# Kernel tuning notes

Measured on AMD Instinct MI355X. Metric: run time of the kernel, lower is better.

The kernel has to match this reference:

```python
import jax, jax.numpy as jnp
import numpy as np

N_E = 4096
E_DIM = 256
DECAY = 0.99
EPS = 1e-5


def setup_inputs() -> dict:
    key = jax.random.key(0)
    k1, k2 = jax.random.split(key)
    z = jax.random.normal(k1, (8, 256, 16, 16, 16), dtype=jnp.float32)
    embedding = jax.random.normal(k2, (N_E, E_DIM), dtype=jnp.float32)
    return {
        "z": z,
        "embedding": embedding,
        "cluster_size": jnp.zeros((N_E,), dtype=jnp.float32),
        "embedding_avg": embedding,  # buffer initialized as embedding.clone()
    }


def reference(z, embedding, cluster_size, embedding_avg):
    n_e, e_dim = embedding.shape
    # b c h w d -> b h w d c, then flatten tokens
    zt = jnp.einsum('bchwd->bhwdc', z)
    zf = zt.reshape(-1, e_dim)                      # [N, e_dim]
    # squared euclidean distances: ||z||^2 + ||e||^2 - 2 z.e
    d = (jnp.sum(zf * zf, axis=1, keepdims=True)
         + jnp.sum(embedding * embedding, axis=1)
         - 2.0 * jnp.einsum('bd,nd->bn', zf, embedding))  # [N, n_e]
    idx = jnp.argmin(d, axis=1)                     # [N]
    # EMA statistics (equivalent to one-hot.T reductions, done via scatter)
    n_total = jnp.zeros((n_e,), zf.dtype).at[idx].add(1.0)          # encodings.sum(0)
    dw = jax.ops.segment_sum(zf, idx, num_segments=n_e)             # encodings.T @ zf
    new_cluster = cluster_size * DECAY + (1.0 - DECAY) * n_total
    new_avg = embedding_avg * DECAY + (1.0 - DECAY) * dw
    n = new_cluster.sum()
    cs = (new_cluster + EPS) / (n + n_e * EPS) * n
    new_embed = new_avg / cs[:, None]
    # quantize (gather == one-hot @ embedding) with straight-through estimator
    zq = jnp.take(embedding, idx, axis=0).reshape(zt.shape)
    zq = zt + jax.lax.stop_gradient(zq - zt)
    zq = jnp.einsum('bhwdc->bchwd', zq)
    usage = (n_total > 0).sum().astype(jnp.float32) / n_e
    return zq, idx, new_cluster, new_avg, new_embed, usage
```

## Files before the change

### kernel.cpp

```cpp
#include <hip/hip_runtime.h>

#define N_E   4096
#define E_DIM 256
#define NTOK  32768
#define ZX    4096
#define DECAY 0.99f
#define EPSV  1e-5f
#define TAU   0.3f
#define NJB   32
#define NSPL  4
#define IBIG  0x7fffffff

typedef _Float16 half8 __attribute__((ext_vector_type(8)));
typedef __attribute__((ext_vector_type(4))) float f32x4;

__device__ __forceinline__ unsigned short f2h(float x) {
    _Float16 h = (_Float16)x;
    unsigned short u;
    __builtin_memcpy(&u, &h, 2);
    return u;
}
__device__ __forceinline__ float h2f(unsigned short u) {
    _Float16 h;
    __builtin_memcpy(&h, &u, 2);
    return (float)h;
}
__device__ __forceinline__ unsigned umin2(unsigned a, unsigned b) { return a < b ? a : b; }
__device__ __forceinline__ unsigned umax2(unsigned a, unsigned b) { return a > b ? a : b; }
__device__ __forceinline__ void gload16(const void* g, void* l) {
    __builtin_amdgcn_global_load_lds(
        (const __attribute__((address_space(1))) char*)g,
        (__attribute__((address_space(3))) char*)l, 16, 0, 0);
}

__global__ void k_prep(const float* __restrict__ z, unsigned short* __restrict__ zh,
                       const float* __restrict__ emb, unsigned short* __restrict__ Bp,
                       float* __restrict__ enorm32, double* __restrict__ enorm64,
                       int* __restrict__ cnt, int* __restrict__ flagCnt,
                       int* __restrict__ flagCnt2) {
    __shared__ float lt[64][65];
    const int tid = threadIdx.x;
    if (blockIdx.x < 2048) {
        const int bid = blockIdx.x;
        const int xt = bid & 63, ct = (bid >> 6) & 3, b = bid >> 8;
        #pragma unroll
        for (int r = 0; r < 4; ++r) {
            int cy = r * 16 + (tid >> 4);
            int xx4 = tid & 15;
            float4 v = ((const float4*)z)[(size_t)(b * 256 + ct * 64 + cy) * 1024 + xt * 16 + xx4];
            lt[cy][xx4 * 4 + 0] = v.x; lt[cy][xx4 * 4 + 1] = v.y;
            lt[cy][xx4 * 4 + 2] = v.z; lt[cy][xx4 * 4 + 3] = v.w;
        }
        __syncthreads();
        #pragma unroll
        for (int it = 0; it < 2; ++it) {
            int tl = it * 32 + (tid >> 3);
            int c8 = tid & 7;
            unsigned short h[8];
            #pragma unroll
            for (int u = 0; u < 8; ++u) h[u] = f2h(lt[c8 * 8 + u][tl]);
            size_t t = (size_t)(b * 4096 + xt * 64 + tl);
            size_t o = t * 256 + ct * 64 + c8 * 8;
            *(ushort4*)&zh[o]     = make_ushort4(h[0], h[1], h[2], h[3]);
            *(ushort4*)&zh[o + 4] = make_ushort4(h[4], h[5], h[6], h[7]);
        }
    } else {
        const int eb = blockIdx.x - 2048;
        if (tid < 4) cnt[eb * 4 + tid] = 0;
        if (eb == 0 && tid == 0) { *flagCnt = 0; *flagCnt2 = 0; }
        int j = eb * 4 + (tid >> 6);
        int lane = tid & 63;
        float4 v = ((const float4*)emb)[(size_t)j * 64 + lane];
        float f[4] = {v.x, v.y, v.z, v.w};
        unsigned short h[4];
        #pragma unroll
        for (int u = 0; u < 4; ++u) h[u] = f2h(f[u]);
        *(ushort4*)&Bp[(size_t)j * E_DIM + lane * 4] = make_ushort4(h[0], h[1], h[2], h[3]);
        double s = 0.0;
        #pragma unroll
        for (int u = 0; u < 4; ++u) s += (double)f[u] * (double)f[u];
        #pragma unroll
        for (int off = 32; off; off >>= 1) s += __shfl_down(s, off, 64);
        if (lane == 0) { enorm32[j] = (float)s; enorm64[j] = s; }
    }
}

__global__ __launch_bounds__(256) void k_dist(
        const unsigned short* __restrict__ zh,
        const unsigned short* __restrict__ Bp, const float* __restrict__ enorm32,
        unsigned* __restrict__ pk1, unsigned* __restrict__ pk2, unsigned* __restrict__ pk3) {
    __shared__ __align__(16) char smem[32768];
    const int tid = threadIdx.x;
    const int lane = tid & 63;
    const int w = tid >> 6;
    const int wr = w >> 1, wc = w & 1;
    const int t0 = blockIdx.x * 128;
    const int jb = blockIdx.y;
    const int j0 = jb * 128;
    const int sw16 = (((lane & 7) ^ (lane >> 3)) << 4);
    const int rowsub = lane >> 3;

    f32x4 acc[4][4];
    #pragma unroll
    for (int m = 0; m < 4; ++m)
        #pragma unroll
        for (int nn = 0; nn < 4; ++nn)
            acc[m][nn] = (f32x4){0.f, 0.f, 0.f, 0.f};

    auto stage = [&](int s) {
        const int kb = s * 128 + sw16;
        #pragma unroll
        for (int c = 0; c < 4; ++c) {
            int seg = w * 4 + c;
            int arow = t0 + seg * 8 + rowsub;
            int brow = j0 + seg * 8 + rowsub;
            gload16((const char*)zh + (size_t)arow * 512 + kb, &smem[seg * 1024]);
            gload16((const char*)Bp + (size_t)brow * 512 + kb, &smem[16384 + seg * 1024]);
        }
    };

    stage(0);
    for (int s = 0; s < 4; ++s) {
        __syncthreads();
        const int xr = ((lane & 7) << 4);
        #pragma unroll
        for (int kk = 0; kk < 2; ++kk) {
            const int colb = (kk * 64 + ((lane >> 4) << 4)) ^ xr;
            half8 a[4], b[4];
            #pragma unroll
            for (int m = 0; m < 4; ++m)
                a[m] = *(const half8*)&smem[((wr * 64 + m * 16 + (lane & 15)) << 7) + colb];
            #pragma unroll
            for (int nn = 0; nn < 4; ++nn)
                b[nn] = *(const half8*)&smem[16384 + ((wc * 64 + nn * 16 + (lane & 15)) << 7) + colb];
            #pragma unroll
            for (int m = 0; m < 4; ++m)
                #pragma unroll
                for (int nn = 0; nn < 4; ++nn)
                    acc[m][nn] = __builtin_amdgcn_mfma_f32_16x16x32_f16(b[nn], a[m], acc[m][nn], 0, 0, 0);
        }
        if (s < 3) {
            __syncthreads();
            stage(s + 1);
        }
    }

    const int g   = lane >> 4;
    const int gg4 = g * 4;
    const int cbase = (wc << 6);
    float enb[4][4];
    #pragma unroll
    for (int nn = 0; nn < 4; ++nn) {
        float4 e4 = *(const float4*)&enorm32[j0 + wc * 64 + nn * 16 + gg4];
        enb[nn][0] = e4.x + 4096.f; enb[nn][1] = e4.y + 4096.f;
        enb[nn][2] = e4.z + 4096.f; enb[nn][3] = e4.w + 4096.f;
    }
    unsigned s1 = 0, s2 = 0, s3 = 0;
    #pragma unroll
    for (int m = 0; m < 4; ++m) {
        unsigned k1 = 0xFFFFFFFFu, k2 = 0xFFFFFFFFu, k3 = 0xFFFFFFFFu;
        #pragma unroll
        for (int nn = 0; nn < 4; ++nn)
            #pragma unroll
            for (int r = 0; r < 4; ++r) {
                float sc = fmaf(-2.f, acc[m][nn][r], enb[nn][r]);
                unsigned key = (__float_as_uint(sc) & 0xFFFFFF80u)
                             | (unsigned)(cbase | (gg4 + nn * 16 + r));
                k3 = umin2(k3, umax2(k2, key));
                k2 = umin2(k2, umax2(k1, key));
                k1 = umin2(k1, key);
            }
        #pragma unroll
        for (int off = 16; off <= 32; off <<= 1) {
            unsigned b1 = (unsigned)__shfl_xor((int)k1, off, 64);
            unsigned b2 = (unsigned)__shfl_xor((int)k2, off, 64);
            unsigned b3 = (unsigned)__shfl_xor((int)k3, off, 64);
            unsigned p  = umax2(k1, b1);
            unsigned q  = umin2(k2, b2);
            unsigned r2 = umax2(k2, b2);
            unsigned ss = umin2(k3, b3);
            k1 = umin2(k1, b1);
            k2 = umin2(p, q);
            k3 = umin2(umax2(p, q), umin2(r2, ss));
        }
        s1 = (g == m) ? k1 : s1;
        s2 = (g == m) ? k2 : s2;
        s3 = (g == m) ? k3 : s3;
    }
    unsigned* mb = (unsigned*)smem;
    __syncthreads();
    if (wc == 1) {
        mb[wr * 64 + lane]       = s1;
        mb[128 + wr * 64 + lane] = s2;
        mb[256 + wr * 64 + lane] = s3;
    }
    __syncthreads();
    if (wc == 0) {
        unsigned o1 = mb[wr * 64 + lane];
        unsigned o2 = mb[128 + wr * 64 + lane];
        unsigned o3 = mb[256 + wr * 64 + lane];
        unsigned r1 = umin2(s1, o1);
        unsigned A  = umax2(s1, o1);
        unsigned B  = umin2(s2, o2);
        unsigned C  = umax2(s2, o2);
        unsigned D  = umin2(s3, o3);
        unsigned r2 = umin2(A, B);
        unsigned r3 = umin2(umax2(A, B), umin2(C, D));
        size_t o = (size_t)jb * NTOK + t0 + wr * 64 + lane;
        pk1[o] = r1; pk2[o] = r2; pk3[o] = r3;
    }
}

__global__ void k_merge(const unsigned* __restrict__ pk1, const unsigned* __restrict__ pk2,
                        const unsigned* __restrict__ pk3,
                        int* __restrict__ idx32, int* __restrict__ cnt,
                        float* __restrict__ out_idx,
                        int* __restrict__ xlist, int* __restrict__ xn,
                        int* __restrict__ flagList, int* __restrict__ flagCount,
                        int* __restrict__ flagList2, int* __restrict__ flagCount2) {
    int t = blockIdx.x * blockDim.x + threadIdx.x;
    if (t >= NTOK) return;
    unsigned g1 = 0xFFFFFFFFu, g2 = 0xFFFFFFFFu;
    int h1 = 0;
    #pragma unroll 4
    for (int s = 0; s < NJB; s++) {
        unsigned a = pk1[(size_t)s * NTOK + t];
        unsigned b = pk2[(size_t)s * NTOK + t];
        bool c = a < g1;
        g2 = c ? g1 : umin2(g2, a);
        h1 = c ? s : h1;
        g1 = c ? a : g1;
        g2 = umin2(g2, b);
    }
    int x1 = h1 * 128 + (int)(g1 & 127u);
    idx32[t] = x1;
    atomicAdd(&cnt[x1], 1);
    out_idx[t] = (float)x1;
    float v1 = __uint_as_float(g1 & 0xFFFFFF80u);
    float v2 = __uint_as_float(g2 & 0xFFFFFF80u);
    if (v2 - v1 >= TAU) return;
    unsigned thrk = __float_as_uint(v1 + TAU) | 127u;
    int nc = 0; bool full = false;
    for (int s = 0; s < NJB; s++) {
        unsigned a = pk1[(size_t)s * NTOK + t];
        if (a > thrk) continue;
        if (pk3[(size_t)s * NTOK + t] <= thrk) { full = true; break; }
        if (nc == 8) { full = true; break; }
        xlist[t * 8 + nc++] = s * 128 + (int)(a & 127u);
        unsigned b = pk2[(size_t)s * NTOK + t];
        if (b <= thrk) {
            if (nc == 8) { full = true; break; }
            xlist[t * 8 + nc++] = s * 128 + (int)(b & 127u);
        }
    }
    if (full) {
        int q = atomicAdd(flagCount2, 1);
        flagList2[q] = t;
    } else {
        xn[t] = nc;
        int q = atomicAdd(flagCount, 1);
        flagList[q] = t;
    }
}

__global__ __launch_bounds__(512) void k_triR(
        const float* __restrict__ z, const float* __restrict__ emb,
        const double* __restrict__ enorm64,
        const int* __restrict__ flagList, const int* __restrict__ flagCount,
        const int* __restrict__ xlist, const int* __restrict__ xn,
        const int* __restrict__ flagList2, const int* __restrict__ flagCount2,
        int* __restrict__ idx32, int* __restrict__ cnt, float* __restrict__ out_idx) {
    __shared__ float zrow[E_DIM];
    __shared__ double rv[512];
    __shared__ int ri[512];
    const int tid = threadIdx.x;
    if (blockIdx.x < 384) {
        const int lane = tid & 63;
        const int wid = blockIdx.x * 8 + (tid >> 6);
        const int nw = 384 * 8;
        const int nf = *flagCount;
        for (int f = wid; f < nf; f += nw) {
            int t = flagList[f];
            int b = t >> 12, x = t & 4095;
            double zz[4];
            #pragma unroll
            for (int u = 0; u < 4; ++u)
                zz[u] = (double)z[(size_t)(b * 256 + lane * 4 + u) * 4096 + x];
            int m = xn[t];
            double best = 1e300; int bi = IBIG;
            for (int c = 0; c < m; ++c) {
                int j = xlist[t * 8 + c];
                float4 e = ((const float4*)emb)[(size_t)j * 64 + lane];
                double d = zz[0] * (double)e.x + zz[1] * (double)e.y
                         + zz[2] * (double)e.z + zz[3] * (double)e.w;
                #pragma unroll
                for (int off = 32; off; off >>= 1) d += __shfl_down(d, off, 64);
                double s = enorm64[j] - 2.0 * d;
                if (s < best || (s == best && j < bi)) { best = s; bi = j; }
            }
            if (lane == 0) {
                int old = idx32[t];
                if (bi != old) {
                    idx32[t] = bi;
                    out_idx[t] = (float)bi;
                    atomicSub(&cnt[old], 1);
                    atomicAdd(&cnt[bi], 1);
                }
            }
        }
    } else {
        const int nf = *flagCount2;
        for (int f = blockIdx.x - 384; f < nf; f += 128) {
            const int t = flagList2[f];
            const int b = t >> 12, x = t & 4095;
            __syncthreads();
            if (tid < E_DIM) zrow[tid] = z[(size_t)(b * 256 + tid) * 4096 + x];
            __syncthreads();
            double best = 1e300; int bi = IBIG;
            for (int s = 0; s < N_E / 512; s++) {
                int j = s * 512 + tid;
                const float4* er4 = (const float4*)(emb + (size_t)j * E_DIM);
                double a0 = 0.0, a1 = 0.0, a2 = 0.0, a3 = 0.0;
                for (int k4 = 0; k4 < 64; ++k4) {
                    float4 e = er4[k4];
                    a0 = fma((double)e.x, (double)zrow[k4 * 4 + 0], a0);
                    a1 = fma((double)e.y, (double)zrow[k4 * 4 + 1], a1);
                    a2 = fma((double)e.z, (double)zrow[k4 * 4 + 2], a2);
                    a3 = fma((double)e.w, (double)zrow[k4 * 4 + 3], a3);
                }
                double d = enorm64[j] - 2.0 * ((a0 + a1) + (a2 + a3));
                if (d < best || (d == best && j < bi)) { best = d; bi = j; }
            }
            rv[tid] = best; ri[tid] = bi;
            __syncthreads();
            for (int off = 256; off; off >>= 1) {
                if (tid < off) {
                    if (rv[tid + off] < rv[tid] ||
                        (rv[tid + off] == rv[tid] && ri[tid + off] < ri[tid])) {
                        rv[tid] = rv[tid + off]; ri[tid] = ri[tid + off];
                    }
                }
                __syncthreads();
            }
            if (tid == 0) {
                int old = idx32[t];
                int nw2 = ri[0];
                if (nw2 != old) {
                    idx32[t] = nw2;
                    out_idx[t] = (float)nw2;
                    atomicSub(&cnt[old], 1);
                    atomicAdd(&cnt[nw2], 1);
                }
            }
            __syncthreads();
        }
    }
}

__global__ void k_scan(const int* __restrict__ cnt, int* __restrict__ offs,
                       const float* __restrict__ cluster_size,
                       float* __restrict__ nval, float* __restrict__ out_usage) {
    __shared__ int sc[1024];
    __shared__ float sn[1024];
    __shared__ float su[1024];
    int tid = threadIdx.x;
    int c0 = cnt[tid * 4], c1 = cnt[tid * 4 + 1], c2 = cnt[tid * 4 + 2], c3 = cnt[tid * 4 + 3];
    int ls = c0 + c1 + c2 + c3;
    float ns = 0.f, us = 0.f;
    {
        int cc[4] = {c0, c1, c2, c3};
        #pragma unroll
        for (int u = 0; u < 4; ++u) {
            ns += cluster_size[tid * 4 + u] * DECAY + (1.f - DECAY) * (float)cc[u];
            us += (cc[u] > 0) ? 1.f : 0.f;
        }
    }
    sc[tid] = ls; sn[tid] = ns; su[tid] = us;
    __syncthreads();
    for (int off = 1; off < 1024; off <<= 1) {
        int v = (tid >= off) ? sc[tid - off] : 0;
        __syncthreads();
        sc[tid] += v;
        __syncthreads();
    }
    int base = sc[tid] - ls;
    offs[tid * 4] = base;
    offs[tid * 4 + 1] = base + c0;
    offs[tid * 4 + 2] = base + c0 + c1;
    offs[tid * 4 + 3] = base + c0 + c1 + c2;
    for (int off = 512; off; off >>= 1) {
        if (tid < off) { sn[tid] += sn[tid + off]; su[tid] += su[tid + off]; }
        __syncthreads();
    }
    if (tid == 0) { *nval = sn[0]; *out_usage = su[0] / (float)N_E; }
}

__global__ void k_place(const int* __restrict__ idx32, int* __restrict__ offs,
                        int* __restrict__ tokList) {
    int t = blockIdx.x * blockDim.x + threadIdx.x;
    if (t >= NTOK) return;
    int j = idx32[t];
    int p = atomicAdd(&offs[j], 1);
    tokList[p] = t;
}

__global__ __launch_bounds__(512) void k_dwzq(const unsigned short* __restrict__ zh,
                       const int* __restrict__ cnt, const int* __restrict__ offs,
                       const int* __restrict__ tokList, float* __restrict__ dwp,
                       const float* __restrict__ emb, const int* __restrict__ idx32,
                       float* __restrict__ out_zq) {
    __shared__ float red[8][256];
    if (blockIdx.x < N_E) {
        const int j = blockIdx.x;
        const int split = blockIdx.y;
        const int g = threadIdx.x >> 6;
        const int lane = threadIdx.x & 63;
        const int n = cnt[j];
        const int s0 = offs[j] - n;
        const int stride = NSPL * 8;
        float4 acc = make_float4(0.f, 0.f, 0.f, 0.f);
        int i = split * 8 + g;
        if (i < n) {
            int t_cur = tokList[s0 + i];
            i += stride;
            for (; i < n; i += stride) {
                int t_nxt = tokList[s0 + i];
                ushort4 h = *(const ushort4*)&zh[(size_t)t_cur * 256 + lane * 4];
                acc.x += h2f(h.x); acc.y += h2f(h.y);
                acc.z += h2f(h.z); acc.w += h2f(h.w);
                t_cur = t_nxt;
            }
            ushort4 h = *(const ushort4*)&zh[(size_t)t_cur * 256 + lane * 4];
            acc.x += h2f(h.x); acc.y += h2f(h.y);
            acc.z += h2f(h.z); acc.w += h2f(h.w);
        }
        red[g][lane * 4 + 0] = acc.x; red[g][lane * 4 + 1] = acc.y;
        red[g][lane * 4 + 2] = acc.z; red[g][lane * 4 + 3] = acc.w;
        __syncthreads();
        if (g == 0) {
            float4 o;
            int c = lane * 4;
            o.x = red[0][c+0] + red[1][c+0] + red[2][c+0] + red[3][c+0]
                + red[4][c+0] + red[5][c+0] + red[6][c+0] + red[7][c+0];
            o.y = red[0][c+1] + red[1][c+1] + red[2][c+1] + red[3][c+1]
                + red[4][c+1] + red[5][c+1] + red[6][c+1] + red[7][c+1];
            o.z = red[0][c+2] + red[1][c+2] + red[2][c+2] + red[3][c+2]
                + red[4][c+2] + red[5][c+2] + red[6][c+2] + red[7][c+2];
            o.w = red[0][c+3] + red[1][c+3] + red[2][c+3] + red[3][c+3]
                + red[4][c+3] + red[5][c+3] + red[6][c+3] + red[7][c+3];
            ((float4*)dwp)[((size_t)split * N_E + j) * 64 + lane] = o;
        }
    } else {
        int t = (blockIdx.x - N_E) * (NSPL * 512) + blockIdx.y * 512 + threadIdx.x;
        int j = idx32[t];
        int b = t >> 12, x = t & 4095;
        const float4* er = (const float4*)(emb + (size_t)j * E_DIM);
        float* ob = out_zq + (size_t)b * (E_DIM * ZX) + x;
        #pragma unroll 8
        for (int c4 = 0; c4 < E_DIM / 4; c4++) {
            float4 v = er[c4];
            ob[(size_t)(c4 * 4 + 0) * ZX] = v.x;
            ob[(size_t)(c4 * 4 + 1) * ZX] = v.y;
            ob[(size_t)(c4 * 4 + 2) * ZX] = v.z;
            ob[(size_t)(c4 * 4 + 3) * ZX] = v.w;
        }
    }
}

__global__ void k_final(const float* __restrict__ dwp, const int* __restrict__ cnt,
                        const float* __restrict__ cluster_size,
                        const float* __restrict__ emb_avg, const float* __restrict__ nval,
                        float* __restrict__ out_cluster, float* __restrict__ out_avg,
                        float* __restrict__ out_embed) {
    int j = blockIdx.x * 4 + (threadIdx.x >> 6);
    int lane = threadIdx.x & 63;
    float4 dw = make_float4(0.f, 0.f, 0.f, 0.f);
    #pragma unroll
    for (int s = 0; s < NSPL; ++s) {
        float4 v = ((const float4*)dwp)[((size_t)s * N_E + j) * 64 + lane];
        dw.x += v.x; dw.y += v.y; dw.z += v.z; dw.w += v.w;
    }
    float nc = cluster_size[j] * DECAY + (1.f - DECAY) * (float)cnt[j];
    float nv = *nval;
    float cs = (nc + EPSV) / (nv + (float)N_E * EPSV) * nv;
    float4 ea = ((const float4*)emb_avg)[(size_t)j * 64 + lane];
    float4 na, ne;
    na.x = ea.x * DECAY + (1.f - DECAY) * dw.x;
    na.y = ea.y * DECAY + (1.f - DECAY) * dw.y;
    na.z = ea.z * DECAY + (1.f - DECAY) * dw.z;
    na.w = ea.w * DECAY + (1.f - DECAY) * dw.w;
    ne.x = na.x / cs; ne.y = na.y / cs; ne.z = na.z / cs; ne.w = na.w / cs;
    ((float4*)out_avg)[(size_t)j * 64 + lane] = na;
    ((float4*)out_embed)[(size_t)j * 64 + lane] = ne;
    if (lane == 0) out_cluster[j] = nc;
}

extern "C" void kernel_launch(void* const* d_in, const int* in_sizes, int n_in,
                              void* d_out, int out_size, void* d_ws, size_t ws_size,
                              hipStream_t stream) {
    const float* z            = (const float*)d_in[0];
    const float* emb          = (const float*)d_in[1];
    const float* cluster_size = (const float*)d_in[2];
    const float* emb_avg      = (const float*)d_in[3];
    float* out = (float*)d_out;

    char* ws = (char*)d_ws;
    unsigned short* zh   = (unsigned short*)(ws + 0);
    float* enorm32       = (float*)(ws + 16777216);
    double* enorm64      = (double*)(ws + 16793600);
    int* idx32           = (int*)(ws + 16826368);
    int* flagList        = (int*)(ws + 16957440);
    int* flagList2       = (int*)(ws + 17088512);
    int* xlist           = (int*)(ws + 17219584);
    int* xn              = (int*)(ws + 18268160);
    int* cnt             = (int*)(ws + 18399232);
    int* offs            = (int*)(ws + 18415616);
    int* flagCnt         = (int*)(ws + 18432000);
    int* flagCnt2        = (int*)(ws + 18432064);
    float* nval          = (float*)(ws + 18432128);
    float* dwp           = (float*)(ws + 18874368);
    int*   tokList       = (int*)(ws + 35651584);

    unsigned* pk1        = (unsigned*)(out + 0);
    unsigned* pk2        = (unsigned*)(out + 1048576);
    unsigned* pk3        = (unsigned*)(out + 2097152);
    unsigned short* Bp   = (unsigned short*)(out + 3145728);

    float* out_zq      = out + 0;
    float* out_idx     = out + 8388608;
    float* out_cluster = out + 8421376;
    float* out_avg     = out + 8425472;
    float* out_embed   = out + 9474048;
    float* out_usage   = out + 10522624;

    hipLaunchKernelGGL(k_prep,   dim3(3072), dim3(256), 0, stream,
                       z, zh, emb, Bp, enorm32, enorm64, cnt, flagCnt, flagCnt2);
    hipLaunchKernelGGL(k_dist,   dim3(256, NJB), dim3(256), 0, stream,
                       zh, Bp, enorm32, pk1, pk2, pk3);
    hipLaunchKernelGGL(k_merge,  dim3(128), dim3(256), 0, stream,
                       pk1, pk2, pk3, idx32, cnt, out_idx,
                       xlist, xn, flagList, flagCnt, flagList2, flagCnt2);
    hipLaunchKernelGGL(k_triR,   dim3(512), dim3(512), 0, stream,
                       z, emb, enorm64, flagList, flagCnt, xlist, xn,
                       flagList2, flagCnt2, idx32, cnt, out_idx);
    hipLaunchKernelGGL(k_scan,   dim3(1), dim3(1024), 0, stream, cnt, offs,
                       cluster_size, nval, out_usage);
    hipLaunchKernelGGL(k_place,  dim3(128), dim3(256), 0, stream, idx32, offs, tokList);
    hipLaunchKernelGGL(k_dwzq,   dim3(N_E + 16, NSPL), dim3(512), 0, stream,
                       zh, cnt, offs, tokList, dwp, emb, idx32, out_zq);
    hipLaunchKernelGGL(k_final,  dim3(1024), dim3(256), 0, stream,
                       dwp, cnt, cluster_size, emb_avg, nval,
                       out_cluster, out_avg, out_embed);
}
```

Measured before the change: 201.8 us.

## Double-buffer distance GEMM K-loop with thinner K-steps and single barrier

Restructures the k_dist main loop from four 128-byte K-stages with two syncthreads each into eight 64-byte K-stages that ping-pong between two 16KB LDS buffers. The next stage is prefetched asynchronously while MFMAs run on the current one, and each iteration ends with one waitcnt plus barrier. The LDS layout and swizzle change so two rows share a 128-byte line. The aim is to overlap global-to-LDS loads with compute and cut barrier count, at the cost of more loop iterations with fewer MFMAs each.

```diff
diff --git a/kernel.cpp b/kernel.cpp
--- a/kernel.cpp
+++ b/kernel.cpp
@@ -97,8 +97,28 @@
     const int t0 = blockIdx.x * 128;
     const int jb = blockIdx.y;
     const int j0 = jb * 128;
-    const int sw16 = (((lane & 7) ^ (lane >> 3)) << 4);
-    const int rowsub = lane >> 3;
+
+    int rowc[2], slotc[2];
+    #pragma unroll
+    for (int c = 0; c < 2; ++c) {
+        int q = c * 256 + tid;
+        int rp = q >> 3, pos = q & 7;
+        int posx = pos ^ (rp & 7);
+        rowc[c] = rp * 2 + (posx >> 2);
+        slotc[c] = posx & 3;
+    }
+    const char* aS0 = (const char*)zh + (size_t)(t0 + rowc[0]) * 512 + slotc[0] * 16;
+    const char* aS1 = (const char*)zh + (size_t)(t0 + rowc[1]) * 512 + slotc[1] * 16;
+    const char* bS0 = (const char*)Bp + (size_t)(j0 + rowc[0]) * 512 + slotc[0] * 16;
+    const char* bS1 = (const char*)Bp + (size_t)(j0 + rowc[1]) * 512 + slotc[1] * 16;
+
+    const int g = lane >> 4;
+    const int r0a = wr * 64 + (lane & 15);
+    const int r0b = wc * 64 + (lane & 15);
+    const int posxA = (g | ((r0a & 1) << 2)) ^ ((r0a >> 1) & 7);
+    const int posxB = (g | ((r0b & 1) << 2)) ^ ((r0b >> 1) & 7);
+    const int Aoff = (r0a >> 1) * 128 + posxA * 16;
+    const int Boff = (r0b >> 1) * 128 + posxB * 16;
 
     f32x4 acc[4][4];
     #pragma unroll
@@ -107,46 +127,40 @@
         for (int nn = 0; nn < 4; ++nn)
             acc[m][nn] = (f32x4){0.f, 0.f, 0.f, 0.f};
 
-    auto stage = [&](int s) {
-        const int kb = s * 128 + sw16;
-        #pragma unroll
-        for (int c = 0; c < 4; ++c) {
-            int seg = w * 4 + c;
-            int arow = t0 + seg * 8 + rowsub;
-            int brow = j0 + seg * 8 + rowsub;
-            gload16((const char*)zh + (size_t)arow * 512 + kb, &smem[seg * 1024]);
-            gload16((const char*)Bp + (size_t)brow * 512 + kb, &smem[16384 + seg * 1024]);
-        }
+    auto stage = [&](int s, int buf) {
+        char* dst = smem + buf * 16384;
+        gload16(aS0 + s * 64, dst + w * 1024);
+        gload16(aS1 + s * 64, dst + 4096 + w * 1024);
+        gload16(bS0 + s * 64, dst + 8192 + w * 1024);
+        gload16(bS1 + s * 64, dst + 12288 + w * 1024);
     };
 
-    stage(0);
-    for (int s = 0; s < 4; ++s) {
-        __syncthreads();
-        const int xr = ((lane & 7) << 4);
-        #pragma unroll
-        for (int kk = 0; kk < 2; ++kk) {
-            const int colb = (kk * 64 + ((lane >> 4) << 4)) ^ xr;
-            half8 a[4], b[4];
-            #pragma unroll
-            for (int m = 0; m < 4; ++m)
-                a[m] = *(const half8*)&smem[((wr * 64 + m * 16 + (lane & 15)) << 7) + colb];
+    stage(0, 0);
+    asm volatile("s_waitcnt vmcnt(0)" ::: "memory");
+    __builtin_amdgcn_s_barrier();
+    #pragma unroll 1
+    for (int s = 0; s < 8; ++s) {
+        const int buf = s & 1;
+        if (s < 7) stage(s + 1, buf ^ 1);
+        const int base = buf * 16384;
+        half8 a[4], b[4];
+        #pragma unroll
+        for (int m = 0; m < 4; ++m)
+            a[m] = *(const half8*)&smem[base + Aoff + m * 1024];
+        #pragma unroll
+        for (int nn = 0; nn < 4; ++nn)
+            b[nn] = *(const half8*)&smem[base + 8192 + Boff + nn * 1024];
+        #pragma unroll
+        for (int m = 0; m < 4; ++m)
             #pragma unroll
             for (int nn = 0; nn < 4; ++nn)
-                b[nn] = *(const half8*)&smem[16384 + ((wc * 64 + nn * 16 + (lane & 15)) << 7) + colb];
-            #pragma unroll
-            for (int m = 0; m < 4; ++m)
-                #pragma unroll
-                for (int nn = 0; nn < 4; ++nn)
-                    acc[m][nn] = __builtin_amdgcn_mfma_f32_16x16x32_f16(b[nn], a[m], acc[m][nn], 0, 0, 0);
-        }
-        if (s < 3) {
-            __syncthreads();
-            stage(s + 1);
-        }
-    }
-
-    const int g   = lane >> 4;
-    const int gg4 = g * 4;
+                acc[m][nn] = __builtin_amdgcn_mfma_f32_16x16x32_f16(b[nn], a[m], acc[m][nn], 0, 0, 0);
+        asm volatile("s_waitcnt vmcnt(0)" ::: "memory");
+        __builtin_amdgcn_s_barrier();
+    }
+
+    const int gq  = lane >> 4;
+    const int gg4 = gq * 4;
     const int cbase = (wc << 6);
     float enb[4][4];
     #pragma unroll
@@ -183,12 +197,11 @@
             k2 = umin2(p, q);
             k3 = umin2(umax2(p, q), umin2(r2, ss));
         }
-        s1 = (g == m) ? k1 : s1;
-        s2 = (g == m) ? k2 : s2;
-        s3 = (g == m) ? k3 : s3;
+        s1 = (gq == m) ? k1 : s1;
+        s2 = (gq == m) ? k2 : s2;
+        s3 = (gq == m) ? k3 : s3;
     }
     unsigned* mb = (unsigned*)smem;
-    __syncthreads();
     if (wc == 1) {
         mb[wr * 64 + lane]       = s1;
         mb[128 + wr * 64 + lane] = s2;
```

Result: slower. 210.8 us (+4.4%).
